# Kernel optimization log

Hardware: AMD Instinct MI355X
Metric: run time of the kernel (lower is better)

The kernel has to match this reference:

```python
import jax, jax.numpy as jnp
import numpy as np

B, N, D, H, DH = 2, 2048, 1024, 16, 64
INNER = H * DH          # 1024
FF_INNER = 4 * D        # 4096 (GEGLU)
EPS = 1e-5


def setup_inputs() -> dict:
    key = jax.random.key(0)
    ks = jax.random.split(key, 12)
    s = D ** -0.5
    return {
        "x": jax.random.normal(ks[0], (B, N, D), jnp.float32),
        "Wq": jax.random.normal(ks[1], (D, INNER), jnp.float32) * s,
        "Wk": jax.random.normal(ks[2], (D, INNER), jnp.float32) * s,
        "Wv": jax.random.normal(ks[3], (D, INNER), jnp.float32) * s,
        "Wo": jax.random.normal(ks[4], (INNER, D), jnp.float32) * s,
        "bo": jnp.zeros((D,), jnp.float32),
        "ln1_g": jnp.ones((D,), jnp.float32),
        "ln1_b": jnp.zeros((D,), jnp.float32),
        "ln3_g": jnp.ones((D,), jnp.float32),
        "ln3_b": jnp.zeros((D,), jnp.float32),
        "Wff1": jax.random.normal(ks[5], (D, 2 * FF_INNER), jnp.float32) * s,
        "bff1": jnp.zeros((2 * FF_INNER,), jnp.float32),
        "Wff2": jax.random.normal(ks[6], (FF_INNER, D), jnp.float32) * (FF_INNER ** -0.5),
        "bff2": jnp.zeros((D,), jnp.float32),
    }


def _layernorm(x, g, b):
    mu = jnp.mean(x, axis=-1, keepdims=True)
    var = jnp.mean(jnp.square(x - mu), axis=-1, keepdims=True)
    return (x - mu) * jax.lax.rsqrt(var + EPS) * g + b


def reference(x, Wq, Wk, Wv, Wo, bo, ln1_g, ln1_b, ln3_g, ln3_b, Wff1, bff1, Wff2, bff2):
    scale = DH ** -0.5

    # norm1 + self-attention (attn1)
    x_features = _layernorm(x, ln1_g, ln1_b)
    q = (x_features @ Wq).reshape(B, N, H, DH)
    k = (x_features @ Wk).reshape(B, N, H, DH)
    v = (x_features @ Wv).reshape(B, N, H, DH)
    sim = jnp.einsum('bihd,bjhd->bhij', q, k) * scale      # (B,H,N,N) full scores
    attn = jax.nn.softmax(sim, axis=-1)
    inter_out = jnp.einsum('bhij,bjhd->bhid', attn, v)     # (B,H,N,DH)
    out = inter_out.transpose(0, 2, 1, 3).reshape(B, N, INNER)
    attended_x = out @ Wo + bo
    x = attended_x + x

    # norm3 + GEGLU feed-forward
    h = _layernorm(x, ln3_g, ln3_b) @ Wff1 + bff1
    a, gate = h[..., :FF_INNER], h[..., FF_INNER:]
    x = (a * jax.nn.gelu(gate, approximate=False)) @ Wff2 + bff2 + x

    # match torch return: q,k,v as (b h) n d, attn = inter_out (b h n d)
    q_bh = q.transpose(0, 2, 1, 3).reshape(B * H, N, DH)
    k_bh = k.transpose(0, 2, 1, 3).reshape(B * H, N, DH)
    v_bh = v.transpose(0, 2, 1, 3).reshape(B * H, N, DH)
    return (x, q_bh, k_bh, v_bh, inter_out, x_features)
```

## Files before the change

### kernel.cpp

```cpp
#include <hip/hip_runtime.h>
#include <hip/hip_bf16.h>

#define B_ 2
#define N_ 2048
#define D_ 1024
#define H_ 16
#define DH_ 64
#define M_ 4096
#define FFI_ 4096

typedef __attribute__((ext_vector_type(8))) short bh8;
typedef __attribute__((ext_vector_type(4))) float f4;

#define DEV static __device__ __forceinline__

DEV short f2bf(float f) { __hip_bfloat16 h = __float2bfloat16(f); return *reinterpret_cast<short*>(&h); }
DEV float bf2f(short s) { __hip_bfloat16 h = *reinterpret_cast<__hip_bfloat16*>(&s); return __bfloat162float(h); }

#define GLDS(gp, lp) __builtin_amdgcn_global_load_lds((const __attribute__((address_space(1))) void*)(gp), (__attribute__((address_space(3))) void*)(lp), 16, 0, 0)
#define MFMA16(a,b,c) __builtin_amdgcn_mfma_f32_16x16x32_bf16(a,b,c,0,0,0)

__global__ __launch_bounds__(256) void ln_kernel(const float* __restrict__ x,
    const float* __restrict__ g, const float* __restrict__ b,
    float* __restrict__ outF, short* __restrict__ outB)
{
  const int row = blockIdx.x;
  const int t = threadIdx.x;
  const float4 v = reinterpret_cast<const float4*>(x + (long)row*D_)[t];
  float s = v.x+v.y+v.z+v.w;
  float sq = v.x*v.x+v.y*v.y+v.z*v.z+v.w*v.w;
  #pragma unroll
  for (int o=32;o>0;o>>=1){ s += __shfl_xor(s,o); sq += __shfl_xor(sq,o); }
  __shared__ float red[8];
  const int w = t>>6, l = t&63;
  if (l==0){ red[w]=s; red[4+w]=sq; }
  __syncthreads();
  s  = red[0]+red[1]+red[2]+red[3];
  sq = red[4]+red[5]+red[6]+red[7];
  const float mu = s*(1.f/D_);
  const float rstd = rsqrtf(sq*(1.f/D_) - mu*mu + 1e-5f);
  const float4 gv = reinterpret_cast<const float4*>(g)[t];
  const float4 bv = reinterpret_cast<const float4*>(b)[t];
  float4 y;
  y.x=(v.x-mu)*rstd*gv.x+bv.x; y.y=(v.y-mu)*rstd*gv.y+bv.y;
  y.z=(v.z-mu)*rstd*gv.z+bv.z; y.w=(v.w-mu)*rstd*gv.w+bv.w;
  if (outF) reinterpret_cast<float4*>(outF + (long)row*D_)[t] = y;
  short4 ys; ys.x=f2bf(y.x); ys.y=f2bf(y.y); ys.z=f2bf(y.z); ys.w=f2bf(y.w);
  reinterpret_cast<short4*>(outB + (long)row*D_)[t] = ys;
}

__global__ __launch_bounds__(256) void transpose_cast(const float* __restrict__ in,
    short* __restrict__ out, int R, int C)
{
  __shared__ float tile[32][33];
  const int tx = threadIdx.x & 31, ty = threadIdx.x >> 5;
  const int c0 = blockIdx.x*32, r0 = blockIdx.y*32;
  #pragma unroll
  for (int i=0;i<4;i++) tile[ty+i*8][tx] = in[(long)(r0+ty+i*8)*C + c0+tx];
  __syncthreads();
  #pragma unroll
  for (int i=0;i<4;i++) out[(long)(c0+ty+i*8)*R + r0+tx] = f2bf(tile[tx][ty+i*8]);
}

DEV void gemm_core(const short* __restrict__ A, const short* __restrict__ BT, int K,
                   int m0, int n0, short* lA, short* lB, f4 (&acc)[4][4])
{
  const int t = threadIdx.x, w = t>>6, l = t&63;
  const int wrow = (w>>1)*64, wcol = (w&1)*64;
  const int lr = l&15, lk = (l>>4)*8;
  const int sr = t>>2, sc = (t&3)*8;
  const short* gA = A  + (long)(m0+sr)*K + sc;
  const short* gB = BT + (long)(n0+sr)*K + sc;
  #pragma unroll
  for (int i=0;i<4;i++)
    #pragma unroll
    for (int j=0;j<4;j++) acc[i][j] = f4{0.f,0.f,0.f,0.f};
  for (int k0=0; k0<K; k0+=32) {
    __syncthreads();
    GLDS(gA,              &lA[w*512]);
    GLDS(gA + (long)64*K, &lA[2048 + w*512]);
    GLDS(gB,              &lB[w*512]);
    GLDS(gB + (long)64*K, &lB[2048 + w*512]);
    gA += 32; gB += 32;
    asm volatile("s_waitcnt vmcnt(0)" ::: "memory");
    __syncthreads();
    bh8 af[4], bf_[4];
    #pragma unroll
    for (int i=0;i<4;i++) af[i]  = *reinterpret_cast<const bh8*>(&lA[(wrow+i*16+lr)*32 + lk]);
    #pragma unroll
    for (int j=0;j<4;j++) bf_[j] = *reinterpret_cast<const bh8*>(&lB[(wcol+j*16+lr)*32 + lk]);
    #pragma unroll
    for (int i=0;i<4;i++)
      #pragma unroll
      for (int j=0;j<4;j++)
        acc[i][j] = MFMA16(af[i], bf_[j], acc[i][j]);
  }
}

__global__ __launch_bounds__(256) void gemm_qkv(const short* __restrict__ A,
    const short* __restrict__ BTq, const short* __restrict__ BTk, const short* __restrict__ BTv,
    float* __restrict__ oQ, float* __restrict__ oK, float* __restrict__ oV,
    short* __restrict__ bQ, short* __restrict__ bK, short* __restrict__ bV)
{
  __shared__ short lA[4096], lB[4096];
  const int m0 = blockIdx.x*128;
  const int by = blockIdx.y, sel = by>>3, n0 = (by&7)*128;
  const short* BT = sel==0 ? BTq : (sel==1 ? BTk : BTv);
  float* oF = sel==0 ? oQ : (sel==1 ? oK : oV);
  short* oB = sel==0 ? bQ : (sel==1 ? bK : bV);
  const float bscale = sel==0 ? 0.125f : 1.0f;
  f4 acc[4][4];
  gemm_core(A, BT, 1024, m0, n0, lA, lB, acc);
  const int t = threadIdx.x, w = t>>6, l = t&63;
  const int wrow=(w>>1)*64, wcol=(w&1)*64, lr=l&15;
  #pragma unroll
  for (int i=0;i<4;i++)
    #pragma unroll
    for (int j=0;j<4;j++)
      #pragma unroll
      for (int r=0;r<4;r++) {
        const int grow = m0 + wrow + i*16 + (l>>4)*4 + r;
        const int gcol = n0 + wcol + j*16 + lr;
        const int bb = grow >> 11, nn = grow & 2047;
        const int hh = gcol >> 6, dd = gcol & 63;
        const long oi = ((long)(bb*H_ + hh)*N_ + nn)*DH_ + dd;
        const float v = acc[i][j][r];
        oF[oi] = v;
        oB[oi] = f2bf(v * bscale);
      }
}

template<int MODE>
__global__ __launch_bounds__(256) void gemm_bt(const short* __restrict__ A,
    const short* __restrict__ BT, int Ndim, int K,
    const float* __restrict__ bias, const float* __restrict__ resid,
    float* __restrict__ outF, short* __restrict__ outB)
{
  __shared__ short lA[4096], lB[4096];
  const int m0 = blockIdx.x*128, n0 = blockIdx.y*128;
  f4 acc[4][4];
  gemm_core(A, BT, K, m0, n0, lA, lB, acc);
  const int t = threadIdx.x, w=t>>6, l=t&63;
  const int wrow=(w>>1)*64, wcol=(w&1)*64, lr=l&15;
  #pragma unroll
  for (int i=0;i<4;i++)
    #pragma unroll
    for (int j=0;j<4;j++)
      #pragma unroll
      for (int r=0;r<4;r++) {
        const int grow = m0 + wrow + i*16 + (l>>4)*4 + r;
        const int gcol = n0 + wcol + j*16 + lr;
        const long oi = (long)grow*Ndim + gcol;
        const float v = acc[i][j][r] + bias[gcol];
        if (MODE==1) outF[oi] = v + resid[oi];
        else         outB[oi] = f2bf(v);
      }
}

__global__ __launch_bounds__(256) void attn_kernel(const short* __restrict__ Q,
    const short* __restrict__ Kb, const short* __restrict__ Vb,
    float* __restrict__ interOut, short* __restrict__ attnB)
{
  __shared__ short Kt[64*64];
  __shared__ short Vt[64*64];
  __shared__ short Pt[4*16*72];
  const int t = threadIdx.x, w = t>>6, l = t&63;
  const int bh = blockIdx.y;
  const int q0 = blockIdx.x*64;
  const int lr = l&15, lk = (l>>4)*8, g = l>>4;
  const long base = (long)bh * (N_*DH_);
  const int qrow = q0 + w*16;
  bh8 qf0 = *reinterpret_cast<const bh8*>(&Q[base + (long)(qrow+lr)*DH_ + lk]);
  bh8 qf1 = *reinterpret_cast<const bh8*>(&Q[base + (long)(qrow+lr)*DH_ + 32 + lk]);
  f4 o[4];
  #pragma unroll
  for (int i=0;i<4;i++) o[i]=f4{0.f,0.f,0.f,0.f};
  float m_run[4], l_run[4];
  #pragma unroll
  for (int r=0;r<4;r++){ m_run[r]=-1e30f; l_run[r]=0.f; }
  short* Pw = &Pt[w*16*72];
  const char* ldsK = (const char*)Kt;
  const int beta0 = w*2048 + l*16;
  const int srow = t>>3, sdp = t&7, sd = sdp*8;
  for (int kt=0; kt<N_/64; kt++) {
    __syncthreads();
    {
      const char* Kg = (const char*)(Kb + base + (long)kt*64*DH_);
      #pragma unroll
      for (int i=0;i<2;i++) {
        const int beta = beta0 + i*1024;
        const int krow = beta>>7, kpch = (beta>>4)&7;
        GLDS(Kg + krow*128 + (kpch ^ (krow&7))*16, (char*)Kt + (w*2+i)*1024);
      }
    }
    #pragma unroll
    for (int it=0; it<2; it++) {
      const int j = it*32 + srow;
      const int4 vv = *reinterpret_cast<const int4*>(&Vb[base + (long)(kt*64+j)*DH_ + sd]);
      const short* vs = reinterpret_cast<const short*>(&vv);
      const int cb0 = (it*4 + (srow>>3)) ^ sdp;
      const int jc  = srow & 7;
      #pragma unroll
      for (int e=0;e<8;e++)
        Vt[(sd+e)*64 + ((cb0^e)<<3) + jc] = vs[e];
    }
    asm volatile("s_waitcnt vmcnt(0)" ::: "memory");
    __syncthreads();
    f4 s[4];
    __builtin_amdgcn_s_setprio(1);
    #pragma unroll
    for (int cb=0;cb<4;cb++) {
      const int krow = cb*16+lr;
      const char* kr = ldsK + krow*128;
      bh8 kf0 = *reinterpret_cast<const bh8*>(kr + ((g  )^(lr&7))*16);
      bh8 kf1 = *reinterpret_cast<const bh8*>(kr + ((g+4)^(lr&7))*16);
      f4 z = f4{0.f,0.f,0.f,0.f};
      z = MFMA16(qf0, kf0, z);
      z = MFMA16(qf1, kf1, z);
      s[cb] = z;
    }
    __builtin_amdgcn_s_setprio(0);
    float mx[4];
    #pragma unroll
    for (int r=0;r<4;r++) mx[r] = fmaxf(fmaxf(s[0][r],s[1][r]), fmaxf(s[2][r],s[3][r]));
    #pragma unroll
    for (int mk=1; mk<16; mk<<=1)
      #pragma unroll
      for (int r=0;r<4;r++) mx[r] = fmaxf(mx[r], __shfl_xor(mx[r], mk));
    float rs[4];
    #pragma unroll
    for (int r=0;r<4;r++) {
      const float mn = fmaxf(m_run[r], mx[r]);
      const float al = __expf(m_run[r]-mn);
      m_run[r] = mn;
      l_run[r] *= al;
      float sum = 0.f;
      #pragma unroll
      for (int cb=0;cb<4;cb++) {
        const float pv = __expf(s[cb][r]-mn);
        sum += pv;
        Pw[((l>>4)*4 + r)*72 + cb*16 + lr] = f2bf(pv);
      }
      rs[r] = sum;
      #pragma unroll
      for (int cb=0;cb<4;cb++) o[cb][r] *= al;
    }
    #pragma unroll
    for (int mk=1; mk<16; mk<<=1)
      #pragma unroll
      for (int r=0;r<4;r++) rs[r] += __shfl_xor(rs[r], mk);
    #pragma unroll
    for (int r=0;r<4;r++) l_run[r] += rs[r];
    asm volatile("s_waitcnt lgkmcnt(0)" ::: "memory");
    __builtin_amdgcn_sched_barrier(0);
    bh8 pa0 = *reinterpret_cast<const bh8*>(&Pw[lr*72 + lk]);
    bh8 pa1 = *reinterpret_cast<const bh8*>(&Pw[lr*72 + 32 + lk]);
    #pragma unroll
    for (int kk=0; kk<2; kk++) {
      const bh8 pa = kk ? pa1 : pa0;
      __builtin_amdgcn_s_setprio(1);
      #pragma unroll
      for (int db=0; db<4; db++) {
        const int dd = db*16 + lr;
        const int ch = (kk*4 + g) ^ (dd&7) ^ ((dd>>3)&7);
        bh8 vf = *reinterpret_cast<const bh8*>(&Vt[dd*64 + ch*8]);
        o[db] = MFMA16(pa, vf, o[db]);
      }
      __builtin_amdgcn_s_setprio(0);
    }
  }
  const int bb = bh>>4, hh = bh&15;
  #pragma unroll
  for (int db=0; db<4; db++)
    #pragma unroll
    for (int r=0;r<4;r++) {
      const int n = qrow + (l>>4)*4 + r;
      const int d = db*16 + lr;
      const float v = o[db][r] / l_run[r];
      interOut[base + (long)n*DH_ + d] = v;
      attnB[(long)(bb*N_ + n)*1024 + hh*DH_ + d] = f2bf(v);
    }
}

__global__ __launch_bounds__(256) void gelu_mul(const short* __restrict__ h, short* __restrict__ g)
{
  const long i = ((long)blockIdx.x*256 + threadIdx.x)*8;
  const long m = i >> 12;
  const int j = (int)(i & 4095);
  bh8 av = *reinterpret_cast<const bh8*>(&h[m*8192 + j]);
  bh8 gv = *reinterpret_cast<const bh8*>(&h[m*8192 + 4096 + j]);
  bh8 ov;
  #pragma unroll
  for (int e=0;e<8;e++) {
    const float a  = bf2f(av[e]);
    const float xg = bf2f(gv[e]);
    const float ge = 0.5f*xg*(1.f + erff(xg*0.70710678118f));
    ov[e] = f2bf(a*ge);
  }
  *reinterpret_cast<bh8*>(&g[i]) = ov;
}

extern "C" void kernel_launch(void* const* d_in, const int* in_sizes, int n_in,
                              void* d_out, int out_size, void* d_ws, size_t ws_size,
                              hipStream_t stream)
{
  const float* x    = (const float*)d_in[0];
  const float* Wq   = (const float*)d_in[1];
  const float* Wk   = (const float*)d_in[2];
  const float* Wv   = (const float*)d_in[3];
  const float* Wo   = (const float*)d_in[4];
  const float* bo   = (const float*)d_in[5];
  const float* ln1g = (const float*)d_in[6];
  const float* ln1b = (const float*)d_in[7];
  const float* ln3g = (const float*)d_in[8];
  const float* ln3b = (const float*)d_in[9];
  const float* Wff1 = (const float*)d_in[10];
  const float* bff1 = (const float*)d_in[11];
  const float* Wff2 = (const float*)d_in[12];
  const float* bff2 = (const float*)d_in[13];
  float* out = (float*)d_out;
  const long SZ = (long)M_*D_;
  float* out_x     = out;
  float* out_q     = out + SZ;
  float* out_k     = out + 2*SZ;
  float* out_v     = out + 3*SZ;
  float* out_inter = out + 4*SZ;
  float* out_xf    = out + 5*SZ;

  char* p = (char*)d_ws;
  auto alloc = [&](size_t bytes){ void* r = (void*)p; p += (bytes + 255) & ~(size_t)255; return r; };
  short* xf_bf  = (short*)alloc(SZ*2);
  short* q_bf   = (short*)alloc(SZ*2);
  short* k_bf   = (short*)alloc(SZ*2);
  short* v_bf   = (short*)alloc(SZ*2);
  short* at_bf  = (short*)alloc(SZ*2);
  float* x2     = (float*)alloc(SZ*4);
  short* x2n_bf = (short*)alloc(SZ*2);
  short* h_bf   = (short*)alloc((size_t)M_*8192*2);
  short* g_bf   = (short*)alloc((size_t)M_*4096*2);
  short* WqT    = (short*)alloc((size_t)1024*1024*2);
  short* WkT    = (short*)alloc((size_t)1024*1024*2);
  short* WvT    = (short*)alloc((size_t)1024*1024*2);
  short* WoT    = (short*)alloc((size_t)1024*1024*2);
  short* Wff1T  = (short*)alloc((size_t)8192*1024*2);
  short* Wff2T  = (short*)alloc((size_t)1024*4096*2);
  (void)in_sizes; (void)n_in; (void)out_size; (void)ws_size;

  dim3 blk(256);
  transpose_cast<<<dim3(32,32),  blk, 0, stream>>>(Wq,   WqT,   1024, 1024);
  transpose_cast<<<dim3(32,32),  blk, 0, stream>>>(Wk,   WkT,   1024, 1024);
  transpose_cast<<<dim3(32,32),  blk, 0, stream>>>(Wv,   WvT,   1024, 1024);
  transpose_cast<<<dim3(32,32),  blk, 0, stream>>>(Wo,   WoT,   1024, 1024);
  transpose_cast<<<dim3(256,32), blk, 0, stream>>>(Wff1, Wff1T, 1024, 8192);
  transpose_cast<<<dim3(32,128), blk, 0, stream>>>(Wff2, Wff2T, 4096, 1024);
  ln_kernel<<<M_, blk, 0, stream>>>(x, ln1g, ln1b, out_xf, xf_bf);
  gemm_qkv<<<dim3(32,24), blk, 0, stream>>>(xf_bf, WqT, WkT, WvT,
                                            out_q, out_k, out_v, q_bf, k_bf, v_bf);
  attn_kernel<<<dim3(32,32), blk, 0, stream>>>(q_bf, k_bf, v_bf, out_inter, at_bf);
  gemm_bt<1><<<dim3(32,8),  blk, 0, stream>>>(at_bf,  WoT,   1024, 1024, bo,   x,   x2,    nullptr);
  ln_kernel<<<M_, blk, 0, stream>>>(x2, ln3g, ln3b, nullptr, x2n_bf);
  gemm_bt<2><<<dim3(32,64), blk, 0, stream>>>(x2n_bf, Wff1T, 8192, 1024, bff1, nullptr, nullptr, h_bf);
  gelu_mul<<<8192, blk, 0, stream>>>(h_bf, g_bf);
  gemm_bt<1><<<dim3(32,8),  blk, 0, stream>>>(g_bf,   Wff2T, 1024, 4096, bff2, x2,  out_x, nullptr);
}
```

Baseline: 611.5 us.

## Double-buffer attention K/V, remap attention blocks, use smaller M tiles for narrow GEMMs

The attention kernel now double-buffers K and V tiles in LDS. The next tile's K loads and V register loads are issued while the current tile is computed. The attention grid is flattened and remapped so consecutive blocks are spread across heads. The output-projection and FF2 GEMMs use 64-row tiles to double the block count (256 to 512), and the four square weight transposes are merged into one launch. These changes target load latency and low occupancy on the 256-block GEMMs, at the cost of extra LDS use and a more complex synchronisation scheme.

```diff
diff --git a/kernel.cpp b/kernel.cpp
--- a/kernel.cpp
+++ b/kernel.cpp
@@ -62,35 +62,56 @@
   for (int i=0;i<4;i++) out[(long)(c0+ty+i*8)*R + r0+tx] = f2bf(tile[tx][ty+i*8]);
 }
 
+__global__ __launch_bounds__(256) void transpose_cast4(
+    const float* __restrict__ i0, const float* __restrict__ i1,
+    const float* __restrict__ i2, const float* __restrict__ i3,
+    short* __restrict__ o0, short* __restrict__ o1,
+    short* __restrict__ o2, short* __restrict__ o3)
+{
+  const int z = blockIdx.z;
+  const float* in = z==0?i0 : z==1?i1 : z==2?i2 : i3;
+  short* out      = z==0?o0 : z==1?o1 : z==2?o2 : o3;
+  __shared__ float tile[32][33];
+  const int tx = threadIdx.x & 31, ty = threadIdx.x >> 5;
+  const int c0 = blockIdx.x*32, r0 = blockIdx.y*32;
+  #pragma unroll
+  for (int i=0;i<4;i++) tile[ty+i*8][tx] = in[(long)(r0+ty+i*8)*1024 + c0+tx];
+  __syncthreads();
+  #pragma unroll
+  for (int i=0;i<4;i++) out[(long)(c0+ty+i*8)*1024 + r0+tx] = f2bf(tile[tx][ty+i*8]);
+}
+
+template<int BM>
 DEV void gemm_core(const short* __restrict__ A, const short* __restrict__ BT, int K,
-                   int m0, int n0, short* lA, short* lB, f4 (&acc)[4][4])
+                   int m0, int n0, short* lA, short* lB, f4 (&acc)[BM/32][4])
 {
   const int t = threadIdx.x, w = t>>6, l = t&63;
-  const int wrow = (w>>1)*64, wcol = (w&1)*64;
+  const int wrow = (w>>1)*(BM/2), wcol = (w&1)*64;
   const int lr = l&15, lk = (l>>4)*8;
   const int sr = t>>2, sc = (t&3)*8;
   const short* gA = A  + (long)(m0+sr)*K + sc;
   const short* gB = BT + (long)(n0+sr)*K + sc;
   #pragma unroll
-  for (int i=0;i<4;i++)
+  for (int i=0;i<BM/32;i++)
     #pragma unroll
     for (int j=0;j<4;j++) acc[i][j] = f4{0.f,0.f,0.f,0.f};
   for (int k0=0; k0<K; k0+=32) {
     __syncthreads();
-    GLDS(gA,              &lA[w*512]);
-    GLDS(gA + (long)64*K, &lA[2048 + w*512]);
+    #pragma unroll
+    for (int i=0;i<BM/64;i++)
+      GLDS(gA + (long)i*64*K, &lA[i*2048 + w*512]);
     GLDS(gB,              &lB[w*512]);
     GLDS(gB + (long)64*K, &lB[2048 + w*512]);
     gA += 32; gB += 32;
     asm volatile("s_waitcnt vmcnt(0)" ::: "memory");
     __syncthreads();
-    bh8 af[4], bf_[4];
-    #pragma unroll
-    for (int i=0;i<4;i++) af[i]  = *reinterpret_cast<const bh8*>(&lA[(wrow+i*16+lr)*32 + lk]);
+    bh8 af[BM/32], bf_[4];
+    #pragma unroll
+    for (int i=0;i<BM/32;i++) af[i] = *reinterpret_cast<const bh8*>(&lA[(wrow+i*16+lr)*32 + lk]);
     #pragma unroll
     for (int j=0;j<4;j++) bf_[j] = *reinterpret_cast<const bh8*>(&lB[(wcol+j*16+lr)*32 + lk]);
     #pragma unroll
-    for (int i=0;i<4;i++)
+    for (int i=0;i<BM/32;i++)
       #pragma unroll
       for (int j=0;j<4;j++)
         acc[i][j] = MFMA16(af[i], bf_[j], acc[i][j]);
@@ -110,7 +131,7 @@
   short* oB = sel==0 ? bQ : (sel==1 ? bK : bV);
   const float bscale = sel==0 ? 0.125f : 1.0f;
   f4 acc[4][4];
-  gemm_core(A, BT, 1024, m0, n0, lA, lB, acc);
+  gemm_core<128>(A, BT, 1024, m0, n0, lA, lB, acc);
   const int t = threadIdx.x, w = t>>6, l = t&63;
   const int wrow=(w>>1)*64, wcol=(w&1)*64, lr=l&15;
   #pragma unroll
@@ -130,20 +151,20 @@
       }
 }
 
-template<int MODE>
+template<int MODE, int BM>
 __global__ __launch_bounds__(256) void gemm_bt(const short* __restrict__ A,
     const short* __restrict__ BT, int Ndim, int K,
     const float* __restrict__ bias, const float* __restrict__ resid,
     float* __restrict__ outF, short* __restrict__ outB)
 {
-  __shared__ short lA[4096], lB[4096];
-  const int m0 = blockIdx.x*128, n0 = blockIdx.y*128;
-  f4 acc[4][4];
-  gemm_core(A, BT, K, m0, n0, lA, lB, acc);
+  __shared__ short lA[BM*32], lB[4096];
+  const int m0 = blockIdx.x*BM, n0 = blockIdx.y*128;
+  f4 acc[BM/32][4];
+  gemm_core<BM>(A, BT, K, m0, n0, lA, lB, acc);
   const int t = threadIdx.x, w=t>>6, l=t&63;
-  const int wrow=(w>>1)*64, wcol=(w&1)*64, lr=l&15;
-  #pragma unroll
-  for (int i=0;i<4;i++)
+  const int wrow=(w>>1)*(BM/2), wcol=(w&1)*64, lr=l&15;
+  #pragma unroll
+  for (int i=0;i<BM/32;i++)
     #pragma unroll
     for (int j=0;j<4;j++)
       #pragma unroll
@@ -161,12 +182,14 @@
     const short* __restrict__ Kb, const short* __restrict__ Vb,
     float* __restrict__ interOut, short* __restrict__ attnB)
 {
-  __shared__ short Kt[64*64];
-  __shared__ short Vt[64*64];
+  __shared__ short Kt[2*64*64];
+  __shared__ short Vt[2*64*64];
   __shared__ short Pt[4*16*72];
   const int t = threadIdx.x, w = t>>6, l = t&63;
-  const int bh = blockIdx.y;
-  const int q0 = blockIdx.x*64;
+  const int bid = blockIdx.x;
+  const int nb = (bid & 7)*128 + (bid >> 3);
+  const int bh = nb >> 5;
+  const int q0 = (nb & 31)*64;
   const int lr = l&15, lk = (l>>4)*8, g = l>>4;
   const long base = (long)bh * (N_*DH_);
   const int qrow = q0 + w*16;
@@ -182,36 +205,52 @@
   const char* ldsK = (const char*)Kt;
   const int beta0 = w*2048 + l*16;
   const int srow = t>>3, sdp = t&7, sd = sdp*8;
-  for (int kt=0; kt<N_/64; kt++) {
-    __syncthreads();
-    {
-      const char* Kg = (const char*)(Kb + base + (long)kt*64*DH_);
+  const int NT = N_/64;
+  int4 vv[2];
+  {
+    const char* Kg = (const char*)(Kb + base);
+    #pragma unroll
+    for (int i=0;i<2;i++) {
+      const int beta = beta0 + i*1024;
+      const int krow = beta>>7, kpch = (beta>>4)&7;
+      GLDS(Kg + krow*128 + (kpch ^ (krow&7))*16, (char*)Kt + (w*2+i)*1024);
+    }
+    #pragma unroll
+    for (int it=0; it<2; it++)
+      vv[it] = *reinterpret_cast<const int4*>(&Vb[base + (long)(it*32+srow)*DH_ + sd]);
+  }
+  for (int kt=0; kt<NT; kt++) {
+    const int b = kt & 1;
+    asm volatile("s_waitcnt vmcnt(0)" ::: "memory");
+    #pragma unroll
+    for (int it=0; it<2; it++) {
+      const short* vs = reinterpret_cast<const short*>(&vv[it]);
+      const int cb0 = (it*4 + (srow>>3)) ^ sdp;
+      const int jc  = srow & 7;
+      #pragma unroll
+      for (int e=0;e<8;e++)
+        Vt[b*4096 + (sd+e)*64 + ((cb0^e)<<3) + jc] = vs[e];
+    }
+    if (kt+1 < NT) {
+      const char* Kg = (const char*)(Kb + base + (long)(kt+1)*64*DH_);
       #pragma unroll
       for (int i=0;i<2;i++) {
         const int beta = beta0 + i*1024;
         const int krow = beta>>7, kpch = (beta>>4)&7;
-        GLDS(Kg + krow*128 + (kpch ^ (krow&7))*16, (char*)Kt + (w*2+i)*1024);
+        GLDS(Kg + krow*128 + (kpch ^ (krow&7))*16, (char*)Kt + (b^1)*8192 + (w*2+i)*1024);
       }
-    }
-    #pragma unroll
-    for (int it=0; it<2; it++) {
-      const int j = it*32 + srow;
-      const int4 vv = *reinterpret_cast<const int4*>(&Vb[base + (long)(kt*64+j)*DH_ + sd]);
-      const short* vs = reinterpret_cast<const short*>(&vv);
-      const int cb0 = (it*4 + (srow>>3)) ^ sdp;
-      const int jc  = srow & 7;
-      #pragma unroll
-      for (int e=0;e<8;e++)
-        Vt[(sd+e)*64 + ((cb0^e)<<3) + jc] = vs[e];
-    }
-    asm volatile("s_waitcnt vmcnt(0)" ::: "memory");
-    __syncthreads();
+      #pragma unroll
+      for (int it=0; it<2; it++)
+        vv[it] = *reinterpret_cast<const int4*>(&Vb[base + (long)((kt+1)*64 + it*32+srow)*DH_ + sd]);
+    }
+    asm volatile("s_waitcnt lgkmcnt(0)" ::: "memory");
+    __builtin_amdgcn_s_barrier();
     f4 s[4];
     __builtin_amdgcn_s_setprio(1);
     #pragma unroll
     for (int cb=0;cb<4;cb++) {
       const int krow = cb*16+lr;
-      const char* kr = ldsK + krow*128;
+      const char* kr = ldsK + b*8192 + krow*128;
       bh8 kf0 = *reinterpret_cast<const bh8*>(kr + ((g  )^(lr&7))*16);
       bh8 kf1 = *reinterpret_cast<const bh8*>(kr + ((g+4)^(lr&7))*16);
       f4 z = f4{0.f,0.f,0.f,0.f};
@@ -263,11 +302,12 @@
       for (int db=0; db<4; db++) {
         const int dd = db*16 + lr;
         const int ch = (kk*4 + g) ^ (dd&7) ^ ((dd>>3)&7);
-        bh8 vf = *reinterpret_cast<const bh8*>(&Vt[dd*64 + ch*8]);
+        bh8 vf = *reinterpret_cast<const bh8*>(&Vt[b*4096 + dd*64 + ch*8]);
         o[db] = MFMA16(pa, vf, o[db]);
       }
       __builtin_amdgcn_s_setprio(0);
     }
+    __builtin_amdgcn_s_barrier();
   }
   const int bb = bh>>4, hh = bh&15;
   #pragma unroll
@@ -347,19 +387,16 @@
   (void)in_sizes; (void)n_in; (void)out_size; (void)ws_size;
 
   dim3 blk(256);
-  transpose_cast<<<dim3(32,32),  blk, 0, stream>>>(Wq,   WqT,   1024, 1024);
-  transpose_cast<<<dim3(32,32),  blk, 0, stream>>>(Wk,   WkT,   1024, 1024);
-  transpose_cast<<<dim3(32,32),  blk, 0, stream>>>(Wv,   WvT,   1024, 1024);
-  transpose_cast<<<dim3(32,32),  blk, 0, stream>>>(Wo,   WoT,   1024, 1024);
+  transpose_cast4<<<dim3(32,32,4), blk, 0, stream>>>(Wq, Wk, Wv, Wo, WqT, WkT, WvT, WoT);
   transpose_cast<<<dim3(256,32), blk, 0, stream>>>(Wff1, Wff1T, 1024, 8192);
   transpose_cast<<<dim3(32,128), blk, 0, stream>>>(Wff2, Wff2T, 4096, 1024);
   ln_kernel<<<M_, blk, 0, stream>>>(x, ln1g, ln1b, out_xf, xf_bf);
   gemm_qkv<<<dim3(32,24), blk, 0, stream>>>(xf_bf, WqT, WkT, WvT,
                                             out_q, out_k, out_v, q_bf, k_bf, v_bf);
-  attn_kernel<<<dim3(32,32), blk, 0, stream>>>(q_bf, k_bf, v_bf, out_inter, at_bf);
-  gemm_bt<1><<<dim3(32,8),  blk, 0, stream>>>(at_bf,  WoT,   1024, 1024, bo,   x,   x2,    nullptr);
+  attn_kernel<<<1024, blk, 0, stream>>>(q_bf, k_bf, v_bf, out_inter, at_bf);
+  gemm_bt<1,64><<<dim3(64,8),  blk, 0, stream>>>(at_bf,  WoT,   1024, 1024, bo,   x,   x2,    nullptr);
   ln_kernel<<<M_, blk, 0, stream>>>(x2, ln3g, ln3b, nullptr, x2n_bf);
-  gemm_bt<2><<<dim3(32,64), blk, 0, stream>>>(x2n_bf, Wff1T, 8192, 1024, bff1, nullptr, nullptr, h_bf);
+  gemm_bt<2,128><<<dim3(32,64), blk, 0, stream>>>(x2n_bf, Wff1T, 8192, 1024, bff1, nullptr, nullptr, h_bf);
   gelu_mul<<<8192, blk, 0, stream>>>(h_bf, g_bf);
-  gemm_bt<1><<<dim3(32,8),  blk, 0, stream>>>(g_bf,   Wff2T, 1024, 4096, bff2, x2,  out_x, nullptr);
-}
+  gemm_bt<1,64><<<dim3(64,8),  blk, 0, stream>>>(g_bf,   Wff2T, 1024, 4096, bff2, x2,  out_x, nullptr);
+}
```

After: 605.0 us. Within noise of the previous version (-1.1%).
